# Performance work log

Measured on AMD Instinct MI355X. Metric: run time of the kernel, lower is better.

The kernel has to match this reference:

```python
import jax, jax.numpy as jnp
import numpy as np

NC, NU, K, C, P, O = 20, 16, 128, 2048, 5, 256

def setup_inputs() -> dict:
    key = jax.random.key(0)
    ks = jax.random.split(key, 6)
    s = 0.02  # keep activations well-scaled
    return {
        "topk_feats": jax.random.normal(ks[0], (NC, NU, K, C), jnp.float32),
        "prototypes": jax.random.normal(ks[1], (NC, P, C), jnp.float32),
        "w_inner1": jax.random.normal(ks[2], (O, C), jnp.float32) * s,
        "w_inner_trans": jax.random.normal(ks[3], (C, C), jnp.float32) * s,
        "w_inter1": jax.random.normal(ks[4], (O, C), jnp.float32) * s,
        "w_inter2": jax.random.normal(ks[5], (O, C), jnp.float32) * s,
    }

def reference(topk_feats, prototypes, w_inner1, w_inner_trans, w_inter1, w_inter2):
    scale = 1.0 / jnp.sqrt(jnp.asarray(O, topk_feats.dtype))
    # --- inner (per-group) self-attention, vmapped over (class, unlabel) ---
    # fe: [nc, nu, k, o]
    fe = jnp.einsum("nukc,oc->nuko", topk_feats, w_inner1)
    att = jax.nn.softmax(jnp.einsum("nuko,nulo->nukl", fe, fe) * scale, axis=-1)
    agg = jnp.einsum("nukl,nulc->nukc", att, topk_feats)  # atte @ feat
    feats = topk_feats + jax.nn.relu(jnp.einsum("nukc,dc->nukd", agg, w_inner_trans))
    # --- inter (prototype -> all feats) cross-attention per class ---
    fa = feats.reshape(NC, NU * K, C)  # cat over unlabel dim
    fae = jnp.einsum("nmc,oc->nmo", fa, w_inter1)
    pe = jnp.einsum("npc,oc->npo", prototypes, w_inter2)
    att2 = jax.nn.softmax(jnp.einsum("npo,nmo->npm", pe, fae) * scale, axis=-1)
    un_protos = jnp.einsum("npm,nmc->npc", att2, fa)  # [nc, p, c]
    return un_protos
```

## Files before the change

### kernel.cpp

```cpp
#include <hip/hip_runtime.h>

typedef __attribute__((ext_vector_type(4))) float f32x4;
typedef __attribute__((ext_vector_type(8))) short short8;

#define DEVI static __device__ __forceinline__

DEVI unsigned short f2bf(float f) {
  unsigned int u = __float_as_uint(f);
  u += 0x7FFFu + ((u >> 16) & 1u);
  return (unsigned short)(u >> 16);
}
DEVI float bf2f(unsigned short s) { return __uint_as_float(((unsigned int)s) << 16); }
DEVI unsigned int pack2(float lo, float hi) {
  return ((unsigned int)f2bf(hi) << 16) | (unsigned int)f2bf(lo);
}

#define GL2LDS(gp, lp)                                                        \
  __builtin_amdgcn_global_load_lds(                                           \
      (const __attribute__((address_space(1))) void*)(const void*)(gp),       \
      (__attribute__((address_space(3))) void*)(void*)(lp), 16, 0, 0)

#define BARRIER __builtin_amdgcn_s_barrier()
#define LGKM0                                                                 \
  do {                                                                        \
    asm volatile("s_waitcnt lgkmcnt(0)" ::: "memory");                        \
    __builtin_amdgcn_sched_barrier(0);                                        \
  } while (0)

__global__ __launch_bounds__(256) void k_cvt_bf16(const float* __restrict__ src,
                                                  unsigned short* __restrict__ dst, int n4) {
  int i = blockIdx.x * 256 + threadIdx.x;
  if (i < n4) {
    float4 v = ((const float4*)src)[i];
    uint2 o; o.x = pack2(v.x, v.y); o.y = pack2(v.z, v.w);
    ((uint2*)dst)[i] = o;
  }
}

template <bool RES>
__global__ __launch_bounds__(256) void k_gemm_bt(const unsigned short* __restrict__ A,
                                                 const unsigned short* __restrict__ B,
                                                 unsigned short* __restrict__ C,
                                                 const float* __restrict__ resid, int N) {
  constexpr int K = 2048;
  __shared__ unsigned short lA[2][128 * 64];
  __shared__ unsigned short lB[2][128 * 64];
  const int tid = threadIdx.x;
  const int lane = tid & 63;
  const int wave = tid >> 6;
  const int wr = wave >> 1, wc = wave & 1;
  const int nx = gridDim.x;
  const int lin = blockIdx.y * nx + blockIdx.x;
  const int cpx = (nx * gridDim.y) >> 3;
  const int swz = (lin & 7) * cpx + (lin >> 3);
  const long mBase = (long)(swz / nx) * 128;
  const long nBase = (long)(swz % nx) * 128;

  f32x4 acc[4][4] = {};

  auto stage = [&](int buf, int k0) {
#pragma unroll
    for (int it = 0; it < 4; it++) {
      int idx = it * 256 + tid;
      int row = idx >> 3, kc = idx & 7;
      int skc = kc ^ (row & 7);
      int lbase = (it * 256 + (tid & ~63)) * 8;
      GL2LDS(A + (mBase + row) * (long)K + k0 + skc * 8, &lA[buf][lbase]);
      GL2LDS(B + (nBase + row) * (long)K + k0 + skc * 8, &lB[buf][lbase]);
    }
  };

  stage(0, 0);
  for (int t = 0; t < 32; t++) {
    const int cur = t & 1;
    if (t < 31) {
      stage(cur ^ 1, (t + 1) * 64);
      asm volatile("s_waitcnt vmcnt(8)" ::: "memory");
    } else {
      asm volatile("s_waitcnt vmcnt(0)" ::: "memory");
    }
    __builtin_amdgcn_s_barrier();
    __builtin_amdgcn_sched_barrier(0);
    const unsigned short* bA = &lA[cur][0];
    const unsigned short* bB = &lB[cur][0];
#pragma unroll
    for (int kb = 0; kb < 2; kb++) {
      short8 af[4], bfr[4];
#pragma unroll
      for (int mt = 0; mt < 4; mt++) {
        int row = wr * 64 + mt * 16 + (lane & 15);
        int slot = (kb * 4 + (lane >> 4)) ^ (row & 7);
        af[mt] = *(const short8*)&bA[row * 64 + slot * 8];
      }
#pragma unroll
      for (int nt = 0; nt < 4; nt++) {
        int row = wc * 64 + nt * 16 + (lane & 15);
        int slot = (kb * 4 + (lane >> 4)) ^ (row & 7);
        bfr[nt] = *(const short8*)&bB[row * 64 + slot * 8];
      }
#pragma unroll
      for (int mt = 0; mt < 4; mt++)
#pragma unroll
        for (int nt = 0; nt < 4; nt++)
          acc[mt][nt] = __builtin_amdgcn_mfma_f32_16x16x32_bf16(af[mt], bfr[nt], acc[mt][nt], 0, 0, 0);
    }
    __builtin_amdgcn_sched_barrier(0);
    __builtin_amdgcn_s_barrier();
  }
#pragma unroll
  for (int mt = 0; mt < 4; mt++) {
#pragma unroll
    for (int nt = 0; nt < 4; nt++) {
#pragma unroll
      for (int j = 0; j < 4; j++) {
        long row = mBase + wr * 64 + mt * 16 + (lane >> 4) * 4 + j;
        long col = nBase + wc * 64 + nt * 16 + (lane & 15);
        float v = acc[mt][nt][j];
        if constexpr (RES) v = resid[row * (long)N + col] + fmaxf(v, 0.0f);
        C[row * (long)N + col] = f2bf(v);
      }
    }
  }
}

template <bool RES>
__global__ __launch_bounds__(512, 1) void k_gemm256_8p(const unsigned short* __restrict__ A,
                                                       const unsigned short* __restrict__ B,
                                                       unsigned short* __restrict__ C,
                                                       const unsigned short* __restrict__ residb,
                                                       int N) {
  constexpr int K = 2048;
  __shared__ unsigned short lA[2][2][128 * 64];
  __shared__ unsigned short lB[2][2][128 * 64];
  const int tid = threadIdx.x;
  const int lane = tid & 63;
  const int wave = tid >> 6;
  const int wr = wave >> 2, wc = wave & 3;
  const int lin = blockIdx.y * 8 + blockIdx.x;
  const int swz = (lin & 7) * 160 + (lin >> 3);
  const long mBase = (long)(swz >> 3) * 256;
  const long nBase = (long)(swz & 7) * 256;

  f32x4 acc[8][4] = {};
  short8 af[4][2];
  short8 bfr[4][2];

  auto stageA = [&](int buf, int half, int t) {
    const unsigned short* base = A + (mBase + half * 128) * (long)K + (long)t * 64;
    unsigned short* lds = &lA[buf][half][0];
#pragma unroll
    for (int it = 0; it < 2; it++) {
      int r = it * 64 + (tid >> 3);
      int kc = tid & 7;
      int skc = kc ^ (r & 7);
      GL2LDS(base + (long)r * K + skc * 8, lds + (it * 512 + (tid & ~63)) * 8);
    }
  };
  auto stageB = [&](int buf, int half, int t) {
    const unsigned short* base = B + (nBase + half * 128) * (long)K + (long)t * 64;
    unsigned short* lds = &lB[buf][half][0];
#pragma unroll
    for (int it = 0; it < 2; it++) {
      int r = it * 64 + (tid >> 3);
      int kc = tid & 7;
      int skc = kc ^ (r & 7);
      GL2LDS(base + (long)r * K + skc * 8, lds + (it * 512 + (tid & ~63)) * 8);
    }
  };
  auto readA = [&](int buf, int mhalf) {
#pragma unroll
    for (int mt = 0; mt < 4; mt++)
#pragma unroll
      for (int kb = 0; kb < 2; kb++) {
        int r = mhalf * 64 + mt * 16 + (lane & 15);
        int slot = (kb * 4 + (lane >> 4)) ^ (r & 7);
        af[mt][kb] = *(const short8*)&lA[buf][wr][r * 64 + slot * 8];
      }
  };
  auto readB = [&](int buf, int nh) {
#pragma unroll
    for (int ntl = 0; ntl < 2; ntl++)
#pragma unroll
      for (int kb = 0; kb < 2; kb++) {
        int nt = nh * 2 + ntl;
        int col = wc * 64 + nt * 16 + (lane & 15);
        int half = col >> 7, r = col & 127;
        int slot = (kb * 4 + (lane >> 4)) ^ (r & 7);
        bfr[nt][kb] = *(const short8*)&lB[buf][half][r * 64 + slot * 8];
      }
  };
  auto mfmaQ = [&](int mhalf, int nh) {
    __builtin_amdgcn_s_setprio(1);
#pragma unroll
    for (int kb = 0; kb < 2; kb++)
#pragma unroll
      for (int mt = 0; mt < 4; mt++)
#pragma unroll
        for (int ntl = 0; ntl < 2; ntl++) {
          int nt = nh * 2 + ntl;
          acc[mhalf * 4 + mt][nt] = __builtin_amdgcn_mfma_f32_16x16x32_bf16(
              af[mt][kb], bfr[nt][kb], acc[mhalf * 4 + mt][nt], 0, 0, 0);
        }
    __builtin_amdgcn_s_setprio(0);
  };

  stageA(0, 0, 0); stageA(0, 1, 0); stageB(0, 0, 0); stageB(0, 1, 0);
  stageA(1, 0, 1); stageA(1, 1, 1); stageB(1, 0, 1); stageB(1, 1, 1);
  asm volatile("s_waitcnt vmcnt(8)" ::: "memory");
  BARRIER;

  for (int t = 0; t < 32; t++) {
    const int cur = t & 1;
    readA(cur, 0);
    readB(cur, 0);
    if (t >= 1 && t <= 30) stageA(cur ^ 1, 1, t + 1);
    BARRIER; LGKM0;
    mfmaQ(0, 0);
    BARRIER;
    readB(cur, 1);
    BARRIER; LGKM0;
    mfmaQ(0, 1);
    BARRIER;
    readA(cur, 1);
    if (t <= 29) stageB(cur, 0, t + 2);
    BARRIER; LGKM0;
    mfmaQ(1, 0);
    BARRIER;
    if (t <= 29) { stageB(cur, 1, t + 2); stageA(cur, 0, t + 2); }
    mfmaQ(1, 1);
    if (t <= 29) {
      asm volatile("s_waitcnt vmcnt(6)" ::: "memory");
    } else if (t == 30) {
      asm volatile("s_waitcnt vmcnt(0)" ::: "memory");
    }
    BARRIER;
  }

#pragma unroll
  for (int mt = 0; mt < 8; mt++) {
#pragma unroll
    for (int nt = 0; nt < 4; nt++) {
#pragma unroll
      for (int j = 0; j < 4; j++) {
        long row = mBase + wr * 128 + mt * 16 + (lane >> 4) * 4 + j;
        long col = nBase + wc * 64 + nt * 16 + (lane & 15);
        float v = acc[mt][nt][j];
        if constexpr (RES) v = bf2f(residb[row * (long)N + col]) + fmaxf(v, 0.0f);
        C[row * (long)N + col] = f2bf(v);
      }
    }
  }
}

__global__ __launch_bounds__(256) void k_attn_inner(const unsigned short* __restrict__ fe,
                                                    const unsigned short* __restrict__ topkb,
                                                    unsigned short* __restrict__ agg) {
  __shared__ unsigned short attb[128 * 136];
  __shared__ unsigned short featT[64 * 128];
  __shared__ float redmax[2 * 128];
  __shared__ float redsum[2 * 128];
  const int tid = threadIdx.x;
  const int lane = tid & 63;
  const int wave = tid >> 6;
  const int wr = wave >> 1, wc = wave & 1;
  const int g = blockIdx.x;
  const unsigned short* feG = fe + (long)g * 128 * 256;

  f32x4 s[4][4] = {};
#pragma unroll
  for (int kb = 0; kb < 8; kb++) {
    short8 af[4], bfr[4];
#pragma unroll
    for (int mt = 0; mt < 4; mt++) {
      int row = wr * 64 + mt * 16 + (lane & 15);
      af[mt] = *(const short8*)(feG + row * 256 + kb * 32 + (lane >> 4) * 8);
    }
#pragma unroll
    for (int nt = 0; nt < 4; nt++) {
      int row = wc * 64 + nt * 16 + (lane & 15);
      bfr[nt] = *(const short8*)(feG + row * 256 + kb * 32 + (lane >> 4) * 8);
    }
#pragma unroll
    for (int mt = 0; mt < 4; mt++)
#pragma unroll
      for (int nt = 0; nt < 4; nt++)
        s[mt][nt] = __builtin_amdgcn_mfma_f32_16x16x32_bf16(af[mt], bfr[nt], s[mt][nt], 0, 0, 0);
  }

  const float cexp = 0.0625f * 1.44269504088896f;
#pragma unroll
  for (int mt = 0; mt < 4; mt++) {
#pragma unroll
    for (int j = 0; j < 4; j++) {
      float m = fmaxf(fmaxf(s[mt][0][j], s[mt][1][j]), fmaxf(s[mt][2][j], s[mt][3][j]));
#pragma unroll
      for (int d = 1; d < 16; d <<= 1) m = fmaxf(m, __shfl_xor(m, d, 64));
      int r = wr * 64 + mt * 16 + (lane >> 4) * 4 + j;
      if ((lane & 15) == 0) redmax[wc * 128 + r] = m;
    }
  }
  __syncthreads();
#pragma unroll
  for (int mt = 0; mt < 4; mt++) {
#pragma unroll
    for (int j = 0; j < 4; j++) {
      int r = wr * 64 + mt * 16 + (lane >> 4) * 4 + j;
      float M = fmaxf(redmax[r], redmax[128 + r]);
      float sm = 0.f;
#pragma unroll
      for (int nt = 0; nt < 4; nt++) {
        float p = exp2f((s[mt][nt][j] - M) * cexp);
        s[mt][nt][j] = p;
        sm += p;
      }
#pragma unroll
      for (int d = 1; d < 16; d <<= 1) sm += __shfl_xor(sm, d, 64);
      if ((lane & 15) == 0) redsum[wc * 128 + r] = sm;
    }
  }
  __syncthreads();
#pragma unroll
  for (int mt = 0; mt < 4; mt++) {
#pragma unroll
    for (int j = 0; j < 4; j++) {
      int r = wr * 64 + mt * 16 + (lane >> 4) * 4 + j;
      float inv = 1.0f / (redsum[r] + redsum[128 + r]);
#pragma unroll
      for (int nt = 0; nt < 4; nt++) {
        int c = wc * 64 + nt * 16 + (lane & 15);
        attb[r * 136 + c] = f2bf(s[mt][nt][j] * inv);
      }
    }
  }

  for (int ch = 0; ch < 32; ch++) {
    __syncthreads();
#pragma unroll
    for (int i = 0; i < 4; i++) {
      int seg = i * 256 + tid;
      int l = seg >> 3, kc = seg & 7;
      const unsigned short* gp = topkb + ((long)g * 128 + l) * 2048 + ch * 64 + kc * 8;
      uint4 w = *(const uint4*)gp;
      unsigned short v[8];
      v[0] = (unsigned short)(w.x & 0xffff); v[1] = (unsigned short)(w.x >> 16);
      v[2] = (unsigned short)(w.y & 0xffff); v[3] = (unsigned short)(w.y >> 16);
      v[4] = (unsigned short)(w.z & 0xffff); v[5] = (unsigned short)(w.z >> 16);
      v[6] = (unsigned short)(w.w & 0xffff); v[7] = (unsigned short)(w.w >> 16);
      int lx = l ^ (kc << 3);
#pragma unroll
      for (int j = 0; j < 8; j++) featT[(kc * 8 + j) * 128 + lx] = v[j];
    }
    __syncthreads();
    f32x4 c[2][4] = {};
#pragma unroll
    for (int kb = 0; kb < 4; kb++) {
      short8 af2[2], bf2v[4];
#pragma unroll
      for (int mt = 0; mt < 2; mt++) {
        int r = wave * 32 + mt * 16 + (lane & 15);
        af2[mt] = *(const short8*)&attb[r * 136 + kb * 32 + (lane >> 4) * 8];
      }
#pragma unroll
      for (int nt = 0; nt < 4; nt++) {
        int cc = nt * 16 + (lane & 15);
        int l0 = (kb * 32 + (lane >> 4) * 8) ^ (((cc >> 3) & 7) << 3);
        bf2v[nt] = *(const short8*)&featT[cc * 128 + l0];
      }
#pragma unroll
      for (int mt = 0; mt < 2; mt++)
#pragma unroll
        for (int nt = 0; nt < 4; nt++)
          c[mt][nt] = __builtin_amdgcn_mfma_f32_16x16x32_bf16(af2[mt], bf2v[nt], c[mt][nt], 0, 0, 0);
    }
#pragma unroll
    for (int mt = 0; mt < 2; mt++)
#pragma unroll
      for (int nt = 0; nt < 4; nt++)
#pragma unroll
        for (int j = 0; j < 4; j++) {
          long row = (long)g * 128 + wave * 32 + mt * 16 + (lane >> 4) * 4 + j;
          int col = ch * 64 + nt * 16 + (lane & 15);
          agg[row * 2048 + col] = f2bf(c[mt][nt][j]);
        }
  }
}

__global__ __launch_bounds__(256) void k_pe(const float* __restrict__ protos,
                                            const float* __restrict__ wi2,
                                            float* __restrict__ pe) {
  int n = blockIdx.x, oc = blockIdx.y, tid = threadIdx.x;
  if (tid < 160) {
    int p = tid >> 5, o = oc * 32 + (tid & 31);
    const float* pr = protos + ((long)n * 5 + p) * 2048;
    const float* wr = wi2 + (long)o * 2048;
    float acc = 0.f;
    for (int cidx = 0; cidx < 2048; cidx += 4) {
      float4 a = *(const float4*)(pr + cidx);
      float4 b = *(const float4*)(wr + cidx);
      acc += a.x * b.x + a.y * b.y + a.z * b.z + a.w * b.w;
    }
    pe[((long)n * 5 + p) * 256 + o] = acc;
  }
}

__global__ __launch_bounds__(256) void k_q(const float* __restrict__ pe,
                                           const float* __restrict__ wi1,
                                           float* __restrict__ q) {
  __shared__ float pel[1280];
  int n = blockIdx.x, cb = blockIdx.y, tid = threadIdx.x;
  for (int i = tid; i < 1280; i += 256) pel[i] = pe[(long)n * 1280 + i];
  __syncthreads();
  int c = cb * 256 + tid;
  float a[5] = {0.f, 0.f, 0.f, 0.f, 0.f};
  for (int o = 0; o < 256; o++) {
    float w = wi1[(long)o * 2048 + c];
#pragma unroll
    for (int p = 0; p < 5; p++) a[p] += pel[p * 256 + o] * w;
  }
#pragma unroll
  for (int p = 0; p < 5; p++) q[((long)n * 5 + p) * 2048 + c] = a[p];
}

__global__ __launch_bounds__(256) void k_lg(const float* __restrict__ q,
                                            const unsigned short* __restrict__ feats,
                                            float* __restrict__ lgp) {
  __shared__ float ql[5 * 1024];
  int n = blockIdx.x, mc = blockIdx.y, cb = blockIdx.z, tid = threadIdx.x;
  const float4* qs = (const float4*)(q + (long)n * 5 * 2048);
  for (int i = tid; i < 1280; i += 256) {
    int p = i >> 8, r = i & 255;
    ((float4*)ql)[i] = qs[p * 512 + cb * 256 + r];
  }
  __syncthreads();
  int m = mc * 256 + tid;
  const unsigned short* fr = feats + ((long)n * 2048 + m) * 2048 + cb * 1024;
  float a[5] = {0.f, 0.f, 0.f, 0.f, 0.f};
  for (int c = 0; c < 1024; c += 8) {
    uint4 w = *(const uint4*)(fr + c);
    float f[8];
    f[0] = bf2f((unsigned short)(w.x & 0xffff)); f[1] = bf2f((unsigned short)(w.x >> 16));
    f[2] = bf2f((unsigned short)(w.y & 0xffff)); f[3] = bf2f((unsigned short)(w.y >> 16));
    f[4] = bf2f((unsigned short)(w.z & 0xffff)); f[5] = bf2f((unsigned short)(w.z >> 16));
    f[6] = bf2f((unsigned short)(w.w & 0xffff)); f[7] = bf2f((unsigned short)(w.w >> 16));
#pragma unroll
    for (int j = 0; j < 8; j++) {
      float fv = f[j];
#pragma unroll
      for (int p = 0; p < 5; p++) a[p] += fv * ql[p * 1024 + c + j];
    }
  }
#pragma unroll
  for (int p = 0; p < 5; p++)
    lgp[((long)cb * 100 + n * 5 + p) * 2048 + m] = a[p] * 0.0625f;
}

__global__ __launch_bounds__(256) void k_sm(const float* __restrict__ lgp,
                                            float* __restrict__ att2) {
  __shared__ float red[4], red2[4];
  int b = blockIdx.x, tid = threadIdx.x;
  const float* s0 = lgp + (long)b * 2048;
  const float* s1 = lgp + (long)100 * 2048 + (long)b * 2048;
  float v[8];
  float mx = -1e30f;
#pragma unroll
  for (int i = 0; i < 8; i++) {
    v[i] = s0[i * 256 + tid] + s1[i * 256 + tid];
    mx = fmaxf(mx, v[i]);
  }
#pragma unroll
  for (int d = 1; d < 64; d <<= 1) mx = fmaxf(mx, __shfl_xor(mx, d, 64));
  if ((tid & 63) == 0) red[tid >> 6] = mx;
  __syncthreads();
  mx = fmaxf(fmaxf(red[0], red[1]), fmaxf(red[2], red[3]));
  float sm = 0.f;
#pragma unroll
  for (int i = 0; i < 8; i++) { v[i] = exp2f((v[i] - mx) * 1.44269504088896f); sm += v[i]; }
#pragma unroll
  for (int d = 1; d < 64; d <<= 1) sm += __shfl_xor(sm, d, 64);
  if ((tid & 63) == 0) red2[tid >> 6] = sm;
  __syncthreads();
  float inv = 1.0f / (red2[0] + red2[1] + red2[2] + red2[3]);
  float* dst = att2 + (long)b * 2048;
#pragma unroll
  for (int i = 0; i < 8; i++) dst[i * 256 + tid] = v[i] * inv;
}

__global__ __launch_bounds__(256) void k_out_part(const float* __restrict__ att2,
                                                  const unsigned short* __restrict__ feats,
                                                  float* __restrict__ partial) {
  __shared__ float a2[5 * 256];
  int n = blockIdx.x, cb = blockIdx.y, ms = blockIdx.z;
  int tid = threadIdx.x;
  const float* src = att2 + (long)n * 5 * 2048 + ms * 256;
  for (int i = tid; i < 320; i += 256) {
    int p = i >> 6, r = i & 63;
    ((float4*)a2)[i] = *(const float4*)(src + p * 2048 + r * 4);
  }
  __syncthreads();
  int c0 = cb * 1024 + tid * 4;
  const unsigned short* fp = feats + ((long)n * 2048 + ms * 256) * 2048 + c0;
  float acc[5][4] = {};
  for (int m = 0; m < 256; m++) {
    uint2 w = *(const uint2*)(fp + (long)m * 2048);
    float f0 = bf2f((unsigned short)(w.x & 0xffff));
    float f1 = bf2f((unsigned short)(w.x >> 16));
    float f2 = bf2f((unsigned short)(w.y & 0xffff));
    float f3 = bf2f((unsigned short)(w.y >> 16));
#pragma unroll
    for (int p = 0; p < 5; p++) {
      float a = a2[p * 256 + m];
      acc[p][0] += a * f0; acc[p][1] += a * f1; acc[p][2] += a * f2; acc[p][3] += a * f3;
    }
  }
  float* pp = partial + ((long)ms * 100 + (long)n * 5) * 2048;
#pragma unroll
  for (int p = 0; p < 5; p++) {
    float4 o; o.x = acc[p][0]; o.y = acc[p][1]; o.z = acc[p][2]; o.w = acc[p][3];
    *(float4*)(pp + p * 2048 + c0) = o;
  }
}

__global__ __launch_bounds__(256) void k_out_red(const float* __restrict__ partial,
                                                 float* __restrict__ outp) {
  int i = blockIdx.x * 256 + threadIdx.x;
  const f32x4* P = (const f32x4*)partial;
  f32x4 s = P[i];
#pragma unroll
  for (int j = 1; j < 8; j++) s += P[(long)j * 51200 + i];
  ((f32x4*)outp)[i] = s;
}

extern "C" void kernel_launch(void* const* d_in, const int* in_sizes, int n_in,
                              void* d_out, int out_size, void* d_ws, size_t ws_size,
                              hipStream_t stream) {
  const float* topk = (const float*)d_in[0];
  const float* protos = (const float*)d_in[1];
  const float* w1 = (const float*)d_in[2];
  const float* wt = (const float*)d_in[3];
  const float* wi1 = (const float*)d_in[4];
  const float* wi2 = (const float*)d_in[5];
  float* outp = (float*)d_out;

  char* ws = (char*)d_ws;
  size_t off = 0;
  auto alloc = [&](size_t bytes) -> void* {
    void* p = ws + off;
    off += (bytes + 255) & ~(size_t)255;
    return p;
  };
  unsigned short* w1b = (unsigned short*)alloc((size_t)256 * 2048 * 2);
  unsigned short* wtb = (unsigned short*)alloc((size_t)2048 * 2048 * 2);
  unsigned short* topkb = (unsigned short*)alloc((size_t)40960 * 2048 * 2);
  unsigned short* fe = (unsigned short*)alloc((size_t)40960 * 256 * 2);
  unsigned short* agg = (unsigned short*)alloc((size_t)40960 * 2048 * 2);
  float* pe = (float*)alloc((size_t)20 * 5 * 256 * 4);
  float* q = (float*)alloc((size_t)20 * 5 * 2048 * 4);
  float* lgp = (float*)alloc((size_t)2 * 100 * 2048 * 4);
  float* att2 = (float*)alloc((size_t)20 * 5 * 2048 * 4);
  float* partial = (float*)alloc((size_t)8 * 100 * 2048 * 4);
  unsigned short* feats = topkb;

  k_cvt_bf16<<<512, 256, 0, stream>>>(w1, w1b, 131072);
  k_cvt_bf16<<<4096, 256, 0, stream>>>(wt, wtb, 1048576);
  k_cvt_bf16<<<81920, 256, 0, stream>>>(topk, topkb, 20971520);

  k_gemm_bt<false><<<dim3(2, 320), 256, 0, stream>>>(topkb, w1b, fe, nullptr, 256);
  k_attn_inner<<<320, 256, 0, stream>>>(fe, topkb, agg);
  k_gemm256_8p<true><<<dim3(8, 160), 512, 0, stream>>>(agg, wtb, feats, topkb, 2048);
  k_pe<<<dim3(20, 8), 256, 0, stream>>>(protos, wi2, pe);
  k_q<<<dim3(20, 8), 256, 0, stream>>>(pe, wi1, q);
  k_lg<<<dim3(20, 8, 2), 256, 0, stream>>>(q, feats, lgp);
  k_sm<<<100, 256, 0, stream>>>(lgp, att2);
  k_out_part<<<dim3(20, 2, 8), 256, 0, stream>>>(att2, feats, partial);
  k_out_red<<<200, 256, 0, stream>>>(partial, outp);
}
```

Baseline: 897.5 us.

## Fuse fp32-to-bf16 conversion of topk features into consuming kernels

Drops the standalone bf16 conversion pass over the large topk feature tensor. The first projection GEMM, the inner attention kernel and the residual epilogue now read fp32 directly and convert on the fly. This removes one full write and read of the bf16 copy and a launch. In exchange, fp32 data is read multiple times, and the projection GEMM loses its asynchronous double-buffered LDS pipeline in favour of synchronous register staging. Residual precision improves since fp32 is used.

```diff
diff --git a/kernel.cpp b/kernel.cpp
--- a/kernel.cpp
+++ b/kernel.cpp
@@ -37,52 +37,40 @@
   }
 }
 
-template <bool RES>
-__global__ __launch_bounds__(256) void k_gemm_bt(const unsigned short* __restrict__ A,
-                                                 const unsigned short* __restrict__ B,
-                                                 unsigned short* __restrict__ C,
-                                                 const float* __restrict__ resid, int N) {
+__global__ __launch_bounds__(256) void k_gemm_f32a(const float* __restrict__ Ap,
+                                                   const unsigned short* __restrict__ B,
+                                                   unsigned short* __restrict__ C, int N) {
   constexpr int K = 2048;
-  __shared__ unsigned short lA[2][128 * 64];
-  __shared__ unsigned short lB[2][128 * 64];
+  __shared__ unsigned short lA[128 * 64];
+  __shared__ unsigned short lB[128 * 64];
   const int tid = threadIdx.x;
   const int lane = tid & 63;
   const int wave = tid >> 6;
   const int wr = wave >> 1, wc = wave & 1;
-  const int nx = gridDim.x;
-  const int lin = blockIdx.y * nx + blockIdx.x;
-  const int cpx = (nx * gridDim.y) >> 3;
-  const int swz = (lin & 7) * cpx + (lin >> 3);
-  const long mBase = (long)(swz / nx) * 128;
-  const long nBase = (long)(swz % nx) * 128;
+  const long mBase = (long)blockIdx.y * 128;
+  const long nBase = (long)blockIdx.x * 128;
 
   f32x4 acc[4][4] = {};
 
-  auto stage = [&](int buf, int k0) {
-#pragma unroll
-    for (int it = 0; it < 4; it++) {
-      int idx = it * 256 + tid;
-      int row = idx >> 3, kc = idx & 7;
-      int skc = kc ^ (row & 7);
-      int lbase = (it * 256 + (tid & ~63)) * 8;
-      GL2LDS(A + (mBase + row) * (long)K + k0 + skc * 8, &lA[buf][lbase]);
-      GL2LDS(B + (nBase + row) * (long)K + k0 + skc * 8, &lB[buf][lbase]);
-    }
-  };
-
-  stage(0, 0);
-  for (int t = 0; t < 32; t++) {
-    const int cur = t & 1;
-    if (t < 31) {
-      stage(cur ^ 1, (t + 1) * 64);
-      asm volatile("s_waitcnt vmcnt(8)" ::: "memory");
-    } else {
-      asm volatile("s_waitcnt vmcnt(0)" ::: "memory");
-    }
-    __builtin_amdgcn_s_barrier();
-    __builtin_amdgcn_sched_barrier(0);
-    const unsigned short* bA = &lA[cur][0];
-    const unsigned short* bB = &lB[cur][0];
+  for (int k0 = 0; k0 < K; k0 += 64) {
+    __syncthreads();
+#pragma unroll
+    for (int i = 0; i < 4; i++) {
+      int seg = i * 256 + tid;
+      int row = seg >> 3;
+      int kc = seg & 7;
+      int slot = kc ^ (row & 7);
+      const float* g = Ap + (mBase + row) * (long)K + k0 + kc * 8;
+      float4 u = *(const float4*)g;
+      float4 v = *(const float4*)(g + 4);
+      uint4 w;
+      w.x = pack2(u.x, u.y); w.y = pack2(u.z, u.w);
+      w.z = pack2(v.x, v.y); w.w = pack2(v.z, v.w);
+      *(uint4*)&lA[row * 64 + slot * 8] = w;
+      const unsigned short* gb = B + (nBase + row) * (long)K + k0 + kc * 8;
+      *(uint4*)&lB[row * 64 + slot * 8] = *(const uint4*)gb;
+    }
+    __syncthreads();
 #pragma unroll
     for (int kb = 0; kb < 2; kb++) {
       short8 af[4], bfr[4];
@@ -90,13 +78,13 @@
       for (int mt = 0; mt < 4; mt++) {
         int row = wr * 64 + mt * 16 + (lane & 15);
         int slot = (kb * 4 + (lane >> 4)) ^ (row & 7);
-        af[mt] = *(const short8*)&bA[row * 64 + slot * 8];
+        af[mt] = *(const short8*)&lA[row * 64 + slot * 8];
       }
 #pragma unroll
       for (int nt = 0; nt < 4; nt++) {
         int row = wc * 64 + nt * 16 + (lane & 15);
         int slot = (kb * 4 + (lane >> 4)) ^ (row & 7);
-        bfr[nt] = *(const short8*)&bB[row * 64 + slot * 8];
+        bfr[nt] = *(const short8*)&lB[row * 64 + slot * 8];
       }
 #pragma unroll
       for (int mt = 0; mt < 4; mt++)
@@ -104,8 +92,6 @@
         for (int nt = 0; nt < 4; nt++)
           acc[mt][nt] = __builtin_amdgcn_mfma_f32_16x16x32_bf16(af[mt], bfr[nt], acc[mt][nt], 0, 0, 0);
     }
-    __builtin_amdgcn_sched_barrier(0);
-    __builtin_amdgcn_s_barrier();
   }
 #pragma unroll
   for (int mt = 0; mt < 4; mt++) {
@@ -115,9 +101,7 @@
       for (int j = 0; j < 4; j++) {
         long row = mBase + wr * 64 + mt * 16 + (lane >> 4) * 4 + j;
         long col = nBase + wc * 64 + nt * 16 + (lane & 15);
-        float v = acc[mt][nt][j];
-        if constexpr (RES) v = resid[row * (long)N + col] + fmaxf(v, 0.0f);
-        C[row * (long)N + col] = f2bf(v);
+        C[row * (long)N + col] = f2bf(acc[mt][nt][j]);
       }
     }
   }
@@ -127,7 +111,7 @@
 __global__ __launch_bounds__(512, 1) void k_gemm256_8p(const unsigned short* __restrict__ A,
                                                        const unsigned short* __restrict__ B,
                                                        unsigned short* __restrict__ C,
-                                                       const unsigned short* __restrict__ residb,
+                                                       const float* __restrict__ resid,
                                                        int N) {
   constexpr int K = 2048;
   __shared__ unsigned short lA[2][2][128 * 64];
@@ -245,7 +229,7 @@
         long row = mBase + wr * 128 + mt * 16 + (lane >> 4) * 4 + j;
         long col = nBase + wc * 64 + nt * 16 + (lane & 15);
         float v = acc[mt][nt][j];
-        if constexpr (RES) v = bf2f(residb[row * (long)N + col]) + fmaxf(v, 0.0f);
+        if constexpr (RES) v = resid[row * (long)N + col] + fmaxf(v, 0.0f);
         C[row * (long)N + col] = f2bf(v);
       }
     }
@@ -253,7 +237,7 @@
 }
 
 __global__ __launch_bounds__(256) void k_attn_inner(const unsigned short* __restrict__ fe,
-                                                    const unsigned short* __restrict__ topkb,
+                                                    const float* __restrict__ topk,
                                                     unsigned short* __restrict__ agg) {
   __shared__ unsigned short attb[128 * 136];
   __shared__ unsigned short featT[64 * 128];
@@ -339,13 +323,12 @@
     for (int i = 0; i < 4; i++) {
       int seg = i * 256 + tid;
       int l = seg >> 3, kc = seg & 7;
-      const unsigned short* gp = topkb + ((long)g * 128 + l) * 2048 + ch * 64 + kc * 8;
-      uint4 w = *(const uint4*)gp;
+      const float* gp = topk + ((long)g * 128 + l) * 2048 + ch * 64 + kc * 8;
+      float4 u = *(const float4*)gp;
+      float4 v2 = *(const float4*)(gp + 4);
       unsigned short v[8];
-      v[0] = (unsigned short)(w.x & 0xffff); v[1] = (unsigned short)(w.x >> 16);
-      v[2] = (unsigned short)(w.y & 0xffff); v[3] = (unsigned short)(w.y >> 16);
-      v[4] = (unsigned short)(w.z & 0xffff); v[5] = (unsigned short)(w.z >> 16);
-      v[6] = (unsigned short)(w.w & 0xffff); v[7] = (unsigned short)(w.w >> 16);
+      v[0] = f2bf(u.x); v[1] = f2bf(u.y); v[2] = f2bf(u.z); v[3] = f2bf(u.w);
+      v[4] = f2bf(v2.x); v[5] = f2bf(v2.y); v[6] = f2bf(v2.z); v[7] = f2bf(v2.w);
       int lx = l ^ (kc << 3);
 #pragma unroll
       for (int j = 0; j < 8; j++) featT[(kc * 8 + j) * 128 + lx] = v[j];
@@ -550,7 +533,7 @@
   };
   unsigned short* w1b = (unsigned short*)alloc((size_t)256 * 2048 * 2);
   unsigned short* wtb = (unsigned short*)alloc((size_t)2048 * 2048 * 2);
-  unsigned short* topkb = (unsigned short*)alloc((size_t)40960 * 2048 * 2);
+  unsigned short* feats = (unsigned short*)alloc((size_t)40960 * 2048 * 2);
   unsigned short* fe = (unsigned short*)alloc((size_t)40960 * 256 * 2);
   unsigned short* agg = (unsigned short*)alloc((size_t)40960 * 2048 * 2);
   float* pe = (float*)alloc((size_t)20 * 5 * 256 * 4);
@@ -558,15 +541,13 @@
   float* lgp = (float*)alloc((size_t)2 * 100 * 2048 * 4);
   float* att2 = (float*)alloc((size_t)20 * 5 * 2048 * 4);
   float* partial = (float*)alloc((size_t)8 * 100 * 2048 * 4);
-  unsigned short* feats = topkb;
 
   k_cvt_bf16<<<512, 256, 0, stream>>>(w1, w1b, 131072);
   k_cvt_bf16<<<4096, 256, 0, stream>>>(wt, wtb, 1048576);
-  k_cvt_bf16<<<81920, 256, 0, stream>>>(topk, topkb, 20971520);
-
-  k_gemm_bt<false><<<dim3(2, 320), 256, 0, stream>>>(topkb, w1b, fe, nullptr, 256);
-  k_attn_inner<<<320, 256, 0, stream>>>(fe, topkb, agg);
-  k_gemm256_8p<true><<<dim3(8, 160), 512, 0, stream>>>(agg, wtb, feats, topkb, 2048);
+
+  k_gemm_f32a<<<dim3(2, 320), 256, 0, stream>>>(topk, w1b, fe, 256);
+  k_attn_inner<<<320, 256, 0, stream>>>(fe, topk, agg);
+  k_gemm256_8p<true><<<dim3(8, 160), 512, 0, stream>>>(agg, wtb, feats, topk, 2048);
   k_pe<<<dim3(20, 8), 256, 0, stream>>>(protos, wi2, pe);
   k_q<<<dim3(20, 8), 256, 0, stream>>>(pe, wi1, q);
   k_lg<<<dim3(20, 8, 2), 256, 0, stream>>>(q, feats, lgp);
```

Result: no change. 899.7 us (+0.2%).
